# Kernel optimization log

Hardware: AMD Instinct MI355X
Metric: run time of the kernel (lower is better)

Reference implementation:

```python
import jax, jax.numpy as jnp
import numpy as np

B, D, L, H, T = 256, 512, 8, 8, 71
DH = D // H
SCALE = 0.01

def _lrelu(x):
    return jax.nn.leaky_relu(x, 0.2)

def _rms(x, dims, w):
    return w * x * jax.lax.rsqrt(jnp.mean(x * x, axis=dims, keepdims=True) + 1e-6)

def _conv(x, w, b, pad):
    y = jax.lax.conv_general_dilated(x, w, (1, 1), pad, dimension_numbers=('NCHW', 'OIHW', 'NCHW'))
    return y + b[None, :, None, None]

def _mha(x, qkv, nw):
    b_, d_, t_ = x.shape
    # einsum 'bdt,nhdD->nbhtD' -> (3,B,H,T,dh)
    y = jnp.einsum('bdt,nhdD->nbhtD', _lrelu(x), qkv)
    y = _rms(y, -2, nw)  # RMSNorm over the token axis (torch dim=-2)
    q, k, v = y[0], y[1], y[2]
    attn = jax.nn.softmax(jnp.einsum('bhtd,bhTd->bhtT', q, k) / np.float32(np.sqrt(DH)), axis=-1)
    out = jnp.einsum('bhtT,bhTd->bhdt', attn, v)  # (B,H,dh,T)
    return out.reshape(b_, d_, t_)

def _convblock(x, w1, b1, w2, b2, nw):
    b_, d_, t_ = x.shape
    y = x.reshape(b_, d_, 8, 8)
    y = _conv(_lrelu(y), w1, b1, 'SAME')
    y = _rms(y, (-1, -2), nw)
    y = _conv(_lrelu(y), w2, b2, 'SAME')
    return y.reshape(b_, d_, t_)

def _forward(fen, move, rank_emb, file_emb, fen_emb, move_emb, abs_emb, ln_w, ln_b, emb_qkv, emb_norm_w, qkv, mha_norm_w, conv1_w, conv1_b, conv2_w, conv2_b, cb_norm_w, out_norm_w, co1_w, co1_b, co2_w, co2_b):
    pos = (rank_emb + file_emb).reshape(64, D)
    mv = (pos[move] + move_emb) * 0.58          # (B,2,D)
    f = fen_emb[fen]                             # (B,133,D)
    board = 0.5 * (f[:, :64] + f[:, 64:128] + pos)
    x = jnp.concatenate([board, f[:, 128:], mv], axis=1) + abs_emb  # (B,71,D)
    x = jnp.swapaxes(x, -1, -2)                  # (B,D,71)
    mu = jnp.mean(x, -1, keepdims=True)
    var = jnp.mean((x - mu) ** 2, -1, keepdims=True)
    x = (x - mu) * jax.lax.rsqrt(var + 1e-5) * ln_w + ln_b  # LayerNorm over T=71
    y = _mha(x, emb_qkv, emb_norm_w)
    x = x[:, :, :64] + y[:, :, :64]              # keep the 64 board squares
    for i in range(L):
        x = x + _convblock(x, conv1_w[i], conv1_b[i], conv2_w[i], conv2_b[i], cb_norm_w[i])
        x = x + _mha(x, qkv[i], mha_norm_w[i])
    x = x.reshape(B, D, 8, 8)
    x = _conv(_lrelu(x), co1_w, co1_b, 'SAME')
    x = _rms(x, (-1, -2), out_norm_w)
    x = _conv(_lrelu(x), co2_w, co2_b, 'VALID')  # (B,1,1,1)
    return x.reshape(-1)

def setup_inputs():
    key = jax.random.key(0)
    ks = jax.random.split(key, 16)
    n = lambda k, s, sc: jax.random.normal(k, s, dtype=jnp.float32) * sc
    return {
        'fen': jax.random.randint(ks[0], (B, 133), 0, 17),
        'move': jax.random.randint(ks[1], (B, 2), 0, 64),
        'rank_emb': n(ks[2], (8, 1, D), SCALE),
        'file_emb': n(ks[3], (1, 8, D), SCALE),
        'fen_emb': n(ks[4], (17, D), SCALE),
        'move_emb': n(ks[5], (2, D), SCALE),
        'abs_emb': n(ks[6], (71, D), SCALE),
        'ln_w': jnp.ones((71,), jnp.float32),
        'ln_b': jnp.zeros((71,), jnp.float32),
        'emb_qkv': n(ks[7], (3, H, D, DH), SCALE),
        'emb_norm_w': jnp.ones((1,), jnp.float32),
        'qkv': n(ks[8], (L, 3, H, D, DH), SCALE * 0.64),
        'mha_norm_w': jnp.ones((L, 1), jnp.float32),
        'conv1_w': n(ks[9], (L, D, D, 3, 3), SCALE * 0.64),
        'conv1_b': jnp.zeros((L, D), jnp.float32),
        'conv2_w': n(ks[10], (L, D, D, 3, 3), SCALE * 0.64),
        'conv2_b': jnp.zeros((L, D), jnp.float32),
        'cb_norm_w': jnp.ones((L, 1), jnp.float32),
        'out_norm_w': jnp.ones((1,), jnp.float32),
        'co1_w': n(ks[11], (2 * D, D, 3, 3), SCALE),
        'co1_b': jnp.zeros((2 * D,), jnp.float32),
        'co2_w': n(ks[12], (1, 2 * D, 8, 8), SCALE),
        'co2_b': jnp.zeros((1,), jnp.float32),
    }

def reference(fen, move, rank_emb, file_emb, fen_emb, move_emb, abs_emb, ln_w, ln_b, emb_qkv, emb_norm_w, qkv, mha_norm_w, conv1_w, conv1_b, conv2_w, conv2_b, cb_norm_w, out_norm_w, co1_w, co1_b, co2_w, co2_b):
    return _forward(fen, move, rank_emb, file_emb, fen_emb, move_emb, abs_emb, ln_w, ln_b, emb_qkv, emb_norm_w, qkv, mha_norm_w, conv1_w, conv1_b, conv2_w, conv2_b, cb_norm_w, out_norm_w, co1_w, co1_b, co2_w, co2_b)
```

## Files before the change

### kernel.cpp

```cpp
#include <hip/hip_runtime.h>
#include <hip/hip_bf16.h>
#include <cstdint>
#include <cstddef>


typedef float f32x4 __attribute__((ext_vector_type(4)));
typedef short short8 __attribute__((ext_vector_type(8)));

__device__ __forceinline__ float lrelu(float v) { return v > 0.f ? v : 0.2f * v; }
__device__ __forceinline__ __hip_bfloat16 tobf(float v) { return __float2bfloat16(v); }
__device__ __forceinline__ float frombf(__hip_bfloat16 v) { return __bfloat162float(v); }

__global__ __launch_bounds__(256) void repack_qkv_w0(
    const float* __restrict__ emb_qkv, __hip_bfloat16* __restrict__ Wq0)
{
  int o = blockIdx.x * 256 + threadIdx.x;
  int j = o >> 9, d = o & 511;
  int n = j >> 9, h = (j >> 6) & 7, dh = j & 63;
  Wq0[o] = tobf(emb_qkv[(((n * 8 + h) * 512 + d) << 6) + dh]);
}

__global__ __launch_bounds__(256) void repack_qkv_w2(
    const float* __restrict__ qkvw, __hip_bfloat16* __restrict__ Wq2)
{
  const int t = blockIdx.x * 256 + threadIdx.x;
  const int lane = t & 63;
  const int nj = (t >> 6) % 96;
  int rest = (t >> 6) / 96;
  const int ks = rest & 1;
  const int kc = (rest >> 1) & 7;
  const int L = rest >> 4;
  const int j = nj * 16 + (lane & 15);
  const int d0 = kc * 64 + ks * 32 + (lane >> 4) * 8;
  const int n = j >> 9, h = (j >> 6) & 7, dh = j & 63;
  const float* src = qkvw + ((((size_t)L * 3 + n) * 8 + h) * 512 + d0) * 64 + dh;
  __hip_bfloat16 tmp[8];
  #pragma unroll
  for (int e = 0; e < 8; ++e) tmp[e] = tobf(src[(size_t)e * 64]);
  *(uint4*)&Wq2[(size_t)t * 8] = *(const uint4*)tmp;
}

__global__ __launch_bounds__(256) void repack_conv_w2(
    const float* __restrict__ w, __hip_bfloat16* __restrict__ W2, int COUT)
{
  const int t = blockIdx.x * 256 + threadIdx.x;
  if (t >= (COUT << 6)) return;
  const int lr = t & 15;
  const int cbg = (t >> 4) & 63;
  const int oj = t >> 10;
  const int cc = cbg >> 3, ks = (cbg >> 2) & 1, lg = cbg & 3;
  const int o = oj * 16 + lr;
  const int NJ = COUT >> 4;
  const float* src = w + ((size_t)o * 512 + cbg * 8) * 9;
  #pragma unroll
  for (int k = 0; k < 9; ++k) {
    __hip_bfloat16 tmp[8];
    #pragma unroll
    for (int e = 0; e < 8; ++e) tmp[e] = tobf(src[e * 9 + k]);
    size_t di = ((((size_t)cc * 9 + k) * NJ + oj) * 2 + ks) * 512 + (lg * 16 + lr) * 8;
    *(uint4*)&W2[di] = *(const uint4*)tmp;
  }
}

__global__ __launch_bounds__(256) void build_ln_kernel(
    const int* __restrict__ fen, const int* __restrict__ move,
    const float* __restrict__ rank_emb, const float* __restrict__ file_emb,
    const float* __restrict__ fen_emb, const float* __restrict__ move_emb,
    const float* __restrict__ abs_emb, const float* __restrict__ lnw,
    const float* __restrict__ lnb, __hip_bfloat16* __restrict__ X71)
{
  const int gid = blockIdx.x * 256 + threadIdx.x;
  const int b = gid >> 9, d = gid & 511;
  const int* fb = fen + b * 133;

  float sum = 0.f, sq = 0.f, mu = 0.f, rstd = 0.f;
  #pragma unroll 1
  for (int pass = 0; pass < 2; ++pass) {
    if (pass) {
      mu = sum * (1.f / 71.f);
      float var = sq * (1.f / 71.f) - mu * mu;
      rstd = rsqrtf(var + 1e-5f);
    }
    #pragma unroll 1
    for (int t = 0; t < 71; ++t) {
      float a = abs_emb[t * 512 + d];
      float v;
      if (t < 64) {
        float pos = rank_emb[(t >> 3) * 512 + d] + file_emb[(t & 7) * 512 + d];
        v = 0.5f * (fen_emb[fb[t] * 512 + d] + fen_emb[fb[64 + t] * 512 + d] + pos) + a;
      } else if (t < 69) {
        v = fen_emb[fb[t + 64] * 512 + d] + a;
      } else {
        int j = t - 69;
        int s = move[b * 2 + j];
        float pos = rank_emb[(s >> 3) * 512 + d] + file_emb[(s & 7) * 512 + d];
        v = (pos + move_emb[j * 512 + d]) * 0.58f + a;
      }
      if (pass) X71[(size_t)gid * 71 + t] = tobf((v - mu) * rstd * lnw[t] + lnb[t]);
      else { sum += v; sq += v * v; }
    }
  }
}

template <int T, int TP>
__global__ __launch_bounds__(256) void proj71_kernel(
    const __hip_bfloat16* __restrict__ xin, const __hip_bfloat16* __restrict__ Wq,
    const float* __restrict__ nw,
    __hip_bfloat16* __restrict__ qk, __hip_bfloat16* __restrict__ vT)
{
  const int b  = blockIdx.x / 6;
  const int jb = (blockIdx.x % 6) * 256;
  const int tid = threadIdx.x;
  const int lane = tid & 63, wv = tid >> 6;
  const int lr = lane & 15, lg = lane >> 4;

  __shared__ __hip_bfloat16 xt[TP * 72];
  __shared__ __hip_bfloat16 wl[256 * 72];

  constexpr int MI = TP / 16;
  f32x4 acc[MI][4];
  #pragma unroll
  for (int mi = 0; mi < MI; ++mi)
    #pragma unroll
    for (int ni = 0; ni < 4; ++ni) acc[mi][ni] = {0.f, 0.f, 0.f, 0.f};

  for (int c0 = 0; c0 < 512; c0 += 64) {
    for (int i = tid; i < 64 * TP; i += 256) {
      int d = i / TP, t = i - d * TP;
      float v = (t < T) ? lrelu(frombf(xin[((size_t)(b * 512 + c0 + d)) * T + t])) : 0.f;
      xt[t * 72 + d] = tobf(v);
    }
    for (int i = tid; i < 2048; i += 256) {
      int j = i >> 3, cb = i & 7;
      *(uint4*)&wl[j * 72 + cb * 8] =
          *(const uint4*)&Wq[(size_t)(jb + j) * 512 + c0 + cb * 8];
    }
    __syncthreads();
    #pragma unroll
    for (int ks = 0; ks < 2; ++ks) {
      short8 a[MI], bb[4];
      #pragma unroll
      for (int mi = 0; mi < MI; ++mi)
        a[mi] = *(const short8*)&xt[(mi * 16 + lr) * 72 + ks * 32 + lg * 8];
      #pragma unroll
      for (int ni = 0; ni < 4; ++ni)
        bb[ni] = *(const short8*)&wl[(wv * 64 + ni * 16 + lr) * 72 + ks * 32 + lg * 8];
      #pragma unroll
      for (int mi = 0; mi < MI; ++mi)
        #pragma unroll
        for (int ni = 0; ni < 4; ++ni)
          acc[mi][ni] = __builtin_amdgcn_mfma_f32_16x16x32_bf16(
              a[mi], bb[ni], acc[mi][ni], 0, 0, 0);
    }
    __syncthreads();
  }

  #pragma unroll
  for (int ni = 0; ni < 4; ++ni) {
    const int j = jb + wv * 64 + ni * 16 + lr;
    float ss = 0.f;
    #pragma unroll
    for (int mi = 0; mi < MI; ++mi)
      #pragma unroll
      for (int r = 0; r < 4; ++r) ss += acc[mi][ni][r] * acc[mi][ni][r];
    ss += __shfl_xor(ss, 16);
    ss += __shfl_xor(ss, 32);
    const float sc = nw[0] * rsqrtf(ss * (1.f / T) + 1e-6f);
    if (j < 1024) {
      #pragma unroll
      for (int mi = 0; mi < MI; ++mi)
        #pragma unroll
        for (int r = 0; r < 4; ++r) {
          int t = mi * 16 + lg * 4 + r;
          if (t < T)
            qk[((size_t)b * T + t) * 1024 + j] = tobf(acc[mi][ni][r] * sc);
        }
    } else {
      const int jj = j - 1024;
      #pragma unroll
      for (int mi = 0; mi < MI; ++mi)
        #pragma unroll
        for (int r = 0; r < 4; ++r) {
          int t = mi * 16 + lg * 4 + r;
          vT[((size_t)b * 512 + jj) * TP + t] = tobf(acc[mi][ni][r] * sc);
        }
    }
  }
}

__global__ __launch_bounds__(256) void proj64_kernel(
    const float* __restrict__ x,
    const __hip_bfloat16* __restrict__ Wq2,
    const float* __restrict__ nw,
    __hip_bfloat16* __restrict__ qk, __hip_bfloat16* __restrict__ vT)
{
  const int b    = blockIdx.x / 6;
  const int jseg = blockIdx.x % 6;
  const int tid = threadIdx.x;
  const int lane = tid & 63, wv = tid >> 6;
  const int lr = lane & 15, lg = lane >> 4;

  __shared__ __hip_bfloat16 xt[2][64 * 72];

  f32x4 acc[4][4];
  #pragma unroll
  for (int mi = 0; mi < 4; ++mi)
    #pragma unroll
    for (int ni = 0; ni < 4; ++ni) acc[mi][ni] = {0.f, 0.f, 0.f, 0.f};

  f32x4 sreg[4];
  const int s_d  = tid >> 4;
  const int s_t4 = (tid & 15) << 2;

  #define PSTAGE_LOAD(kc_)                                                    \
    {                                                                         \
      const float* xb_ = x + ((size_t)b * 512 + (kc_) * 64 + s_d) * 64 + s_t4; \
      _Pragma("unroll")                                                       \
      for (int u = 0; u < 4; ++u) sreg[u] = *(const f32x4*)&xb_[u * 1024];    \
    }
  #define PSTAGE_WRITE(buf_)                                                  \
    {                                                                         \
      _Pragma("unroll")                                                       \
      for (int u = 0; u < 4; ++u) {                                           \
        _Pragma("unroll")                                                     \
        for (int j = 0; j < 4; ++j)                                           \
          xt[buf_][(s_t4 + j) * 72 + s_d + u * 16] = tobf(lrelu(sreg[u][j])); \
      }                                                                       \
    }

  PSTAGE_LOAD(0);
  PSTAGE_WRITE(0);
  __syncthreads();

  const int njb0 = jseg * 16 + wv * 4;

  for (int kc = 0; kc < 8; ++kc) {
    const int cur = kc & 1;
    if (kc < 7) PSTAGE_LOAD(kc + 1);
    const __hip_bfloat16* xb = xt[cur];
    #pragma unroll
    for (int ks = 0; ks < 2; ++ks) {
      short8 bv[4], av[4];
      #pragma unroll
      for (int ni = 0; ni < 4; ++ni)
        bv[ni] = *(const short8*)
            &Wq2[((((size_t)kc * 2 + ks) * 96) + njb0 + ni) * 512 + lane * 8];
      #pragma unroll
      for (int mi = 0; mi < 4; ++mi)
        av[mi] = *(const short8*)&xb[(mi * 16 + lr) * 72 + ks * 32 + lg * 8];
      #pragma unroll
      for (int mi = 0; mi < 4; ++mi)
        #pragma unroll
        for (int ni = 0; ni < 4; ++ni)
          acc[mi][ni] = __builtin_amdgcn_mfma_f32_16x16x32_bf16(
              av[mi], bv[ni], acc[mi][ni], 0, 0, 0);
    }
    if (kc < 7) PSTAGE_WRITE(cur ^ 1);
    __syncthreads();
  }
  #undef PSTAGE_LOAD
  #undef PSTAGE_WRITE

  #pragma unroll
  for (int ni = 0; ni < 4; ++ni) {
    const int j = jseg * 256 + wv * 64 + ni * 16 + lr;
    float ss = 0.f;
    #pragma unroll
    for (int mi = 0; mi < 4; ++mi)
      #pragma unroll
      for (int r = 0; r < 4; ++r) ss += acc[mi][ni][r] * acc[mi][ni][r];
    ss += __shfl_xor(ss, 16);
    ss += __shfl_xor(ss, 32);
    const float sc = nw[0] * rsqrtf(ss * (1.f / 64.f) + 1e-6f);
    if (j < 1024) {
      #pragma unroll
      for (int mi = 0; mi < 4; ++mi)
        #pragma unroll
        for (int r = 0; r < 4; ++r) {
          int t = mi * 16 + lg * 4 + r;
          qk[((size_t)b * 64 + t) * 1024 + j] = tobf(acc[mi][ni][r] * sc);
        }
    } else {
      const int jj = j - 1024;
      #pragma unroll
      for (int mi = 0; mi < 4; ++mi)
        #pragma unroll
        for (int r = 0; r < 4; ++r) {
          int t = mi * 16 + lg * 4 + r;
          vT[((size_t)b * 512 + jj) * 64 + t] = tobf(acc[mi][ni][r] * sc);
        }
    }
  }
}

template <int T, bool RESBF>
__global__ __launch_bounds__(256) void attn2_kernel(
    const __hip_bfloat16* __restrict__ qk,
    const __hip_bfloat16* __restrict__ vT,
    const void* __restrict__ res, float* __restrict__ out)
{
  constexpr int TP = (T == 71) ? 80 : 64;
  constexpr int TK = (T + 31) / 32;
  constexpr int RS = 72;
  constexpr int PS = TK * 32 + 8;
  constexpr int KR = (T == 71) ? 80 : 64;
  constexpr int SC = (T == 71) ? 82 : 66;
  constexpr int NCF = KR / 16;
  constexpr int NFW = (NCF + 3) / 4;
  constexpr int RANGE = (TK * 32) / 4;

  constexpr int Q_OFF = 0;
  constexpr int K_OFF = Q_OFF + 64 * RS * 2;
  constexpr int V_OFF = K_OFF + KR * RS * 2;
  constexpr int S_OFF = V_OFF + 64 * PS * 2;
  constexpr int BYTES = S_OFF + 64 * SC * 4;
  __shared__ __align__(16) char smem[BYTES];
  __hip_bfloat16* qs = (__hip_bfloat16*)(smem + Q_OFF);
  __hip_bfloat16* ksh = (__hip_bfloat16*)(smem + K_OFF);
  __hip_bfloat16* vs = (__hip_bfloat16*)(smem + V_OFF);
  float* ss = (float*)(smem + S_OFF);
  __hip_bfloat16* ps = (__hip_bfloat16*)(smem + S_OFF);

  const int b = blockIdx.x >> 3, h = blockIdx.x & 7;
  const int tid = threadIdx.x;
  const int lane = tid & 63, wv = tid >> 6;
  const int lr = lane & 15, lg = lane >> 4;

  for (int i = tid; i < BYTES / 16; i += 256) ((uint4*)smem)[i] = uint4{0, 0, 0, 0};
  __syncthreads();

  const __hip_bfloat16* qb = qk + (size_t)b * T * 1024 + h * 64;
  for (int v = tid; v < 512; v += 256) {
    int t = v >> 3, d0 = (v & 7) * 8;
    *(uint4*)&qs[t * RS + d0] = *(const uint4*)&qb[(size_t)t * 1024 + d0];
  }
  for (int v = tid; v < T * 8; v += 256) {
    int t = v >> 3, d0 = (v & 7) * 8;
    *(uint4*)&ksh[t * RS + d0] = *(const uint4*)&qb[(size_t)t * 1024 + 512 + d0];
  }
  constexpr int VV = TP / 8;
  for (int v = tid; v < 64 * VV; v += 256) {
    int dh = v / VV, tc = (v - dh * VV) * 8;
    *(uint4*)&vs[dh * PS + tc] =
        *(const uint4*)&vT[((size_t)b * 512 + h * 64 + dh) * TP + tc];
  }
  __syncthreads();

  f32x4 sacc[NFW][4];
  #pragma unroll
  for (int fi = 0; fi < NFW; ++fi)
    #pragma unroll
    for (int mi = 0; mi < 4; ++mi) sacc[fi][mi] = {0.f, 0.f, 0.f, 0.f};
  #pragma unroll
  for (int ks2 = 0; ks2 < 2; ++ks2) {
    short8 a[4];
    #pragma unroll
    for (int mi = 0; mi < 4; ++mi)
      a[mi] = *(const short8*)&qs[(mi * 16 + lr) * RS + ks2 * 32 + lg * 8];
    #pragma unroll
    for (int fi = 0; fi < NFW; ++fi) {
      const int f = wv + fi * 4;
      if (f < NCF) {
        short8 bb = *(const short8*)&ksh[(f * 16 + lr) * RS + ks2 * 32 + lg * 8];
        #pragma unroll
        for (int mi = 0; mi < 4; ++mi)
          sacc[fi][mi] = __builtin_amdgcn_mfma_f32_16x16x32_bf16(
              a[mi], bb, sacc[fi][mi], 0, 0, 0);
      }
    }
  }
  #pragma unroll
  for (int fi = 0; fi < NFW; ++fi) {
    const int f = wv + fi * 4;
    if (f < NCF) {
      #pragma unroll
      for (int mi = 0; mi < 4; ++mi)
        #pragma unroll
        for (int r = 0; r < 4; ++r)
          ss[(mi * 16 + lg * 4 + r) * SC + f * 16 + lr] = sacc[fi][mi][r] * 0.125f;
    }
  }
  __syncthreads();

  {
    const int row = tid >> 2, q4 = tid & 3;
    float sv[RANGE];
    float mx = -3.0e38f;
    #pragma unroll
    for (int i = 0; i < RANGE; ++i) {
      int c = q4 * RANGE + i;
      sv[i] = (c < T) ? ss[row * SC + c] : -3.0e38f;
      mx = fmaxf(mx, sv[i]);
    }
    mx = fmaxf(mx, __shfl_xor(mx, 1));
    mx = fmaxf(mx, __shfl_xor(mx, 2));
    float sm = 0.f;
    #pragma unroll
    for (int i = 0; i < RANGE; ++i) {
      int c = q4 * RANGE + i;
      sv[i] = (c < T) ? __expf(sv[i] - mx) : 0.f;
      sm += sv[i];
    }
    sm += __shfl_xor(sm, 1);
    sm += __shfl_xor(sm, 2);
    const float inv = 1.f / sm;
    __syncthreads();
    #pragma unroll
    for (int i = 0; i < RANGE; ++i)
      ps[row * PS + q4 * RANGE + i] = tobf(sv[i] * inv);
  }
  __syncthreads();

  f32x4 oacc[4];
  #pragma unroll
  for (int mi = 0; mi < 4; ++mi) oacc[mi] = {0.f, 0.f, 0.f, 0.f};
  #pragma unroll
  for (int ks2 = 0; ks2 < TK; ++ks2) {
    short8 bb = *(const short8*)&vs[(wv * 16 + lr) * PS + ks2 * 32 + lg * 8];
    #pragma unroll
    for (int mi = 0; mi < 4; ++mi) {
      short8 a = *(const short8*)&ps[(mi * 16 + lr) * PS + ks2 * 32 + lg * 8];
      oacc[mi] = __builtin_amdgcn_mfma_f32_16x16x32_bf16(a, bb, oacc[mi], 0, 0, 0);
    }
  }

  const int dh = wv * 16 + lr;
  const size_t chb = (size_t)b * 512 + h * 64 + dh;
  #pragma unroll
  for (int mi = 0; mi < 4; ++mi) {
    const int t0 = mi * 16 + lg * 4;
    const size_t idx = chb * 64 + t0;
    f32x4 v = oacc[mi];
    if constexpr (RESBF) {
      const __hip_bfloat16* rb = (const __hip_bfloat16*)res + chb * T + t0;
      #pragma unroll
      for (int r = 0; r < 4; ++r) v[r] += frombf(rb[r]);
    } else {
      v += *(const f32x4*)&((const float*)res)[idx];
    }
    *(f32x4*)&out[idx] = v;
  }
}

template <bool RMSOUT, bool RESADD>
__global__ __launch_bounds__(256) void conv_mfma2(
    const float* __restrict__ x,
    const __hip_bfloat16* __restrict__ W2,
    const float* __restrict__ bias,
    const float* __restrict__ nw,
    const float* __restrict__ res,
    float* __restrict__ out,
    int COUT)
{
  const int ntc = COUT >> 8;
  const int b = blockIdx.x / ntc;
  const int nt = blockIdx.x - b * ntc;
  const int o0 = nt << 8;
  const int NJ = COUT >> 4;
  const int tid = threadIdx.x;
  const int lane = tid & 63, wv = tid >> 6;
  const int lr = lane & 15, lg = lane >> 4;

  __shared__ __hip_bfloat16 xt[2][100 * 72];

  f32x4 acc[4][4];
  #pragma unroll
  for (int mi = 0; mi < 4; ++mi)
    #pragma unroll
    for (int ni = 0; ni < 4; ++ni) acc[mi][ni] = {0.f, 0.f, 0.f, 0.f};

  for (int i = tid; i < 7200; i += 256) { xt[0][i] = tobf(0.f); xt[1][i] = tobf(0.f); }

  f32x4 sreg[4];
  const int s_ci = tid >> 4;
  const int s_p4 = (tid & 15) << 2;
  const int s_row = (((s_p4 >> 3) + 1) * 10 + (s_p4 & 7) + 1) * 72;

  #define STAGE_LOAD(cc_)                                                     \
    {                                                                         \
      const float* xb_ = x + ((size_t)b * 512 + (cc_) * 64 + s_ci) * 64 + s_p4; \
      _Pragma("unroll")                                                       \
      for (int u = 0; u < 4; ++u) sreg[u] = *(const f32x4*)&xb_[u * 1024];    \
    }
  #define STAGE_WRITE(buf_)                                                   \
    {                                                                         \
      _Pragma("unroll")                                                       \
      for (int u = 0; u < 4; ++u) {                                           \
        _Pragma("unroll")                                                     \
        for (int j = 0; j < 4; ++j)                                           \
          xt[buf_][s_row + j * 72 + s_ci + u * 16] = tobf(lrelu(sreg[u][j])); \
      }                                                                       \
    }

  STAGE_LOAD(0);
  __syncthreads();
  STAGE_WRITE(0);
  __syncthreads();

  const int ojb2 = ((o0 >> 4) + wv * 4) * 2;

  for (int cc = 0; cc < 8; ++cc) {
    const int cur = cc & 1;
    if (cc < 7) STAGE_LOAD(cc + 1);
    const __hip_bfloat16* xb = xt[cur];

    #pragma unroll
    for (int k = 0; k < 9; ++k) {
      const int dy = k / 3 - 1, dx = k - (k / 3) * 3 - 1;
      const int ii0 = (lr >> 3) + dy + 1;
      const int jj0 = (lr & 7) + dx + 1;
      const size_t slab = ((size_t)(cc * 9 + k) * NJ) * 2 + ojb2;
      short8 bv[2][4], av[2][4];
      #pragma unroll
      for (int ni = 0; ni < 4; ++ni)
        #pragma unroll
        for (int ks = 0; ks < 2; ++ks)
          bv[ks][ni] = *(const short8*)&W2[(slab + ni * 2 + ks) * 512 + lane * 8];
      #pragma unroll
      for (int ks = 0; ks < 2; ++ks)
        #pragma unroll
        for (int mi = 0; mi < 4; ++mi)
          av[ks][mi] = *(const short8*)&xb[((ii0 + mi * 2) * 10 + jj0) * 72 + ks * 32 + lg * 8];
      #pragma unroll
      for (int ks = 0; ks < 2; ++ks)
        #pragma unroll
        for (int mi = 0; mi < 4; ++mi)
          #pragma unroll
          for (int ni = 0; ni < 4; ++ni)
            acc[mi][ni] = __builtin_amdgcn_mfma_f32_16x16x32_bf16(
                av[ks][mi], bv[ks][ni], acc[mi][ni], 0, 0, 0);
    }
    if (cc < 7) STAGE_WRITE(cur ^ 1);
    __syncthreads();
  }
  #undef STAGE_LOAD
  #undef STAGE_WRITE

  #pragma unroll
  for (int ni = 0; ni < 4; ++ni) {
    const int o = o0 + wv * 64 + ni * 16 + lr;
    const float bvs = bias[o];
    float sc = 1.f;
    if constexpr (RMSOUT) {
      float ssq = 0.f;
      #pragma unroll
      for (int mi = 0; mi < 4; ++mi)
        #pragma unroll
        for (int r = 0; r < 4; ++r) {
          float v = acc[mi][ni][r] + bvs;
          ssq += v * v;
        }
      ssq += __shfl_xor(ssq, 16);
      ssq += __shfl_xor(ssq, 32);
      sc = nw[0] * rsqrtf(ssq * (1.f / 64.f) + 1e-6f);
    }
    #pragma unroll
    for (int mi = 0; mi < 4; ++mi) {
      size_t idx = ((size_t)b * COUT + o) * 64 + mi * 16 + lg * 4;
      f32x4 v;
      #pragma unroll
      for (int r = 0; r < 4; ++r) v[r] = (acc[mi][ni][r] + bvs) * sc;
      if constexpr (RESADD) v += *(const f32x4*)&res[idx];
      *(f32x4*)&out[idx] = v;
    }
  }
}

__global__ __launch_bounds__(256) void co2_kernel(
    const float* __restrict__ xf, const float* __restrict__ w,
    const float* __restrict__ cb, float* __restrict__ out)
{
  const int b = blockIdx.x, tid = threadIdx.x;
  const float* xb = xf + (size_t)b * 65536;
  float acc = 0.f;
  for (int i = tid; i < 65536; i += 256)
    acc += lrelu(xb[i]) * w[i];
  #pragma unroll
  for (int off = 32; off; off >>= 1) acc += __shfl_down(acc, off);
  __shared__ float red[4];
  if ((tid & 63) == 0) red[tid >> 6] = acc;
  __syncthreads();
  if (tid == 0) out[b] = red[0] + red[1] + red[2] + red[3] + cb[0];
}

extern "C" void kernel_launch(void* const* d_in, const int* in_sizes, int n_in,
                              void* d_out, int out_size, void* d_ws, size_t ws_size,
                              hipStream_t stream)
{
  const int*   fen        = (const int*)d_in[0];
  const int*   move       = (const int*)d_in[1];
  const float* rank_emb   = (const float*)d_in[2];
  const float* file_emb   = (const float*)d_in[3];
  const float* fen_emb    = (const float*)d_in[4];
  const float* move_emb   = (const float*)d_in[5];
  const float* abs_emb    = (const float*)d_in[6];
  const float* ln_w       = (const float*)d_in[7];
  const float* ln_b       = (const float*)d_in[8];
  const float* emb_qkv    = (const float*)d_in[9];
  const float* emb_norm_w = (const float*)d_in[10];
  const float* qkvw_in    = (const float*)d_in[11];
  const float* mha_norm_w = (const float*)d_in[12];
  const float* conv1_w    = (const float*)d_in[13];
  const float* conv1_b    = (const float*)d_in[14];
  const float* conv2_w    = (const float*)d_in[15];
  const float* conv2_b    = (const float*)d_in[16];
  const float* cb_norm_w  = (const float*)d_in[17];
  const float* out_norm_w = (const float*)d_in[18];
  const float* co1_w      = (const float*)d_in[19];
  const float* co1_b      = (const float*)d_in[20];
  const float* co2_w      = (const float*)d_in[21];
  const float* co2_b      = (const float*)d_in[22];
  float* out = (float*)d_out;

  char* base = (char*)d_ws;
  __hip_bfloat16* X71 = (__hip_bfloat16*)base;
  float* X64 = (float*)(base + 18612224);
  float* T1  = (float*)(base + 18612224 + 33554432);
  __hip_bfloat16* Wq0 = (__hip_bfloat16*)(base + 119275520);
  __hip_bfloat16* Wq2 = (__hip_bfloat16*)(base + 120848384);
  __hip_bfloat16* qk2 = (__hip_bfloat16*)T1;
  __hip_bfloat16* vTb = (__hip_bfloat16*)((char*)T1 + 37224448);
  float* F1 = T1;
  __hip_bfloat16* WcA = (__hip_bfloat16*)base;
  __hip_bfloat16* WcB = (__hip_bfloat16*)(base + 4718592);

  repack_qkv_w0<<<3072, 256, 0, stream>>>(emb_qkv, Wq0);
  repack_qkv_w2<<<3072, 256, 0, stream>>>(qkvw_in, Wq2);

  build_ln_kernel<<<512, 256, 0, stream>>>(fen, move, rank_emb, file_emb,
                                           fen_emb, move_emb, abs_emb,
                                           ln_w, ln_b, X71);
  proj71_kernel<71, 80><<<1536, 256, 0, stream>>>(X71, Wq0, emb_norm_w, qk2, vTb);
  attn2_kernel<71, true><<<2048, 256, 0, stream>>>(qk2, vTb, X71, X64);

  for (int l = 0; l < 8; ++l) {
    repack_conv_w2<<<128, 256, 0, stream>>>(conv1_w + (size_t)l * 512 * 512 * 9,
                                            WcA, 512);
    conv_mfma2<true, false><<<512, 256, 0, stream>>>(X64, WcA, conv1_b + l * 512,
                                                     cb_norm_w + l, nullptr, T1, 512);
    repack_conv_w2<<<128, 256, 0, stream>>>(conv2_w + (size_t)l * 512 * 512 * 9,
                                            WcB, 512);
    conv_mfma2<false, true><<<512, 256, 0, stream>>>(T1, WcB, conv2_b + l * 512,
                                                     nullptr, X64, X64, 512);
    proj64_kernel<<<1536, 256, 0, stream>>>(X64, Wq2 + (size_t)l * 786432,
                                            mha_norm_w + l, qk2, vTb);
    attn2_kernel<64, false><<<2048, 256, 0, stream>>>(qk2, vTb, X64, X64);
  }

  repack_conv_w2<<<256, 256, 0, stream>>>(co1_w, WcA, 1024);
  conv_mfma2<true, false><<<1024, 256, 0, stream>>>(X64, WcA, co1_b,
                                                    out_norm_w, nullptr, F1, 1024);
  co2_kernel<<<256, 256, 0, stream>>>(F1, co2_w, co2_b, out);
}
```

Baseline: 2.690 ms.

## Tile conv and projection kernels over two batch samples per block

Each conv block now handles two batch samples and 128 output channels instead of one sample and 256 channels, so every weight fragment loaded from global memory feeds twice as many MFMAs. The QKV projection kernel is likewise changed to process two samples per block, halving its grid. The two per-layer conv weight repacks are merged into a single launch. The cost is doubled shared memory per block for the staged inputs, plus more registers holding input fragments, which may reduce occupancy.

```diff
diff --git a/kernel.cpp b/kernel.cpp
--- a/kernel.cpp
+++ b/kernel.cpp
@@ -58,6 +58,30 @@
     #pragma unroll
     for (int e = 0; e < 8; ++e) tmp[e] = tobf(src[e * 9 + k]);
     size_t di = ((((size_t)cc * 9 + k) * NJ + oj) * 2 + ks) * 512 + (lg * 16 + lr) * 8;
+    *(uint4*)&W2[di] = *(const uint4*)tmp;
+  }
+}
+
+__global__ __launch_bounds__(256) void repack_conv_pair(
+    const float* __restrict__ w1, const float* __restrict__ w2s,
+    __hip_bfloat16* __restrict__ WA, __hip_bfloat16* __restrict__ WB)
+{
+  int t = blockIdx.x * 256 + threadIdx.x;
+  const float* w = (t < 32768) ? w1 : w2s;
+  __hip_bfloat16* W2 = (t < 32768) ? WA : WB;
+  t &= 32767;
+  const int lr = t & 15;
+  const int cbg = (t >> 4) & 63;
+  const int oj = t >> 10;
+  const int cc = cbg >> 3, ks = (cbg >> 2) & 1, lg = cbg & 3;
+  const int o = oj * 16 + lr;
+  const float* src = w + ((size_t)o * 512 + cbg * 8) * 9;
+  #pragma unroll
+  for (int k = 0; k < 9; ++k) {
+    __hip_bfloat16 tmp[8];
+    #pragma unroll
+    for (int e = 0; e < 8; ++e) tmp[e] = tobf(src[e * 9 + k]);
+    size_t di = ((((size_t)cc * 9 + k) * 32 + oj) * 2 + ks) * 512 + (lg * 16 + lr) * 8;
     *(uint4*)&W2[di] = *(const uint4*)tmp;
   }
 }
@@ -188,44 +212,52 @@
   }
 }
 
-__global__ __launch_bounds__(256) void proj64_kernel(
+__global__ __launch_bounds__(256) void proj64b_kernel(
     const float* __restrict__ x,
     const __hip_bfloat16* __restrict__ Wq2,
     const float* __restrict__ nw,
     __hip_bfloat16* __restrict__ qk, __hip_bfloat16* __restrict__ vT)
 {
-  const int b    = blockIdx.x / 6;
-  const int jseg = blockIdx.x % 6;
+  const int jseg = blockIdx.x >> 7;
+  const int bg   = blockIdx.x & 127;
+  const int b0   = bg * 2;
   const int tid = threadIdx.x;
   const int lane = tid & 63, wv = tid >> 6;
   const int lr = lane & 15, lg = lane >> 4;
 
-  __shared__ __hip_bfloat16 xt[2][64 * 72];
-
-  f32x4 acc[4][4];
-  #pragma unroll
-  for (int mi = 0; mi < 4; ++mi)
+  __shared__ __hip_bfloat16 xt[2][2][64 * 72];
+
+  f32x4 acc[8][4];
+  #pragma unroll
+  for (int mi = 0; mi < 8; ++mi)
     #pragma unroll
     for (int ni = 0; ni < 4; ++ni) acc[mi][ni] = {0.f, 0.f, 0.f, 0.f};
 
-  f32x4 sreg[4];
+  f32x4 sreg[2][4];
   const int s_d  = tid >> 4;
   const int s_t4 = (tid & 15) << 2;
 
-  #define PSTAGE_LOAD(kc_)                                                    \
-    {                                                                         \
-      const float* xb_ = x + ((size_t)b * 512 + (kc_) * 64 + s_d) * 64 + s_t4; \
-      _Pragma("unroll")                                                       \
-      for (int u = 0; u < 4; ++u) sreg[u] = *(const f32x4*)&xb_[u * 1024];    \
-    }
-  #define PSTAGE_WRITE(buf_)                                                  \
-    {                                                                         \
-      _Pragma("unroll")                                                       \
-      for (int u = 0; u < 4; ++u) {                                           \
-        _Pragma("unroll")                                                     \
-        for (int j = 0; j < 4; ++j)                                           \
-          xt[buf_][(s_t4 + j) * 72 + s_d + u * 16] = tobf(lrelu(sreg[u][j])); \
-      }                                                                       \
+  #define PSTAGE_LOAD(kc_)                                                      \
+    {                                                                           \
+      _Pragma("unroll")                                                         \
+      for (int s = 0; s < 2; ++s) {                                             \
+        const float* xb_ =                                                      \
+            x + ((size_t)(b0 + s) * 512 + (kc_) * 64 + s_d) * 64 + s_t4;        \
+        _Pragma("unroll")                                                       \
+        for (int u = 0; u < 4; ++u) sreg[s][u] = *(const f32x4*)&xb_[u * 1024]; \
+      }                                                                         \
+    }
+  #define PSTAGE_WRITE(buf_)                                                    \
+    {                                                                           \
+      _Pragma("unroll")                                                         \
+      for (int s = 0; s < 2; ++s)                                               \
+        _Pragma("unroll")                                                       \
+        for (int u = 0; u < 4; ++u) {                                           \
+          _Pragma("unroll")                                                     \
+          for (int j = 0; j < 4; ++j)                                           \
+            xt[buf_][s][(s_t4 + j) * 72 + s_d + u * 16] =                       \
+                tobf(lrelu(sreg[s][u][j]));                                     \
+        }                                                                       \
     }
 
   PSTAGE_LOAD(0);
@@ -237,19 +269,19 @@
   for (int kc = 0; kc < 8; ++kc) {
     const int cur = kc & 1;
     if (kc < 7) PSTAGE_LOAD(kc + 1);
-    const __hip_bfloat16* xb = xt[cur];
     #pragma unroll
     for (int ks = 0; ks < 2; ++ks) {
-      short8 bv[4], av[4];
+      short8 bv[4], av[8];
       #pragma unroll
       for (int ni = 0; ni < 4; ++ni)
         bv[ni] = *(const short8*)
             &Wq2[((((size_t)kc * 2 + ks) * 96) + njb0 + ni) * 512 + lane * 8];
       #pragma unroll
-      for (int mi = 0; mi < 4; ++mi)
-        av[mi] = *(const short8*)&xb[(mi * 16 + lr) * 72 + ks * 32 + lg * 8];
-      #pragma unroll
-      for (int mi = 0; mi < 4; ++mi)
+      for (int mi = 0; mi < 8; ++mi)
+        av[mi] = *(const short8*)
+            &xt[cur][mi >> 2][((mi & 3) * 16 + lr) * 72 + ks * 32 + lg * 8];
+      #pragma unroll
+      for (int mi = 0; mi < 8; ++mi)
         #pragma unroll
         for (int ni = 0; ni < 4; ++ni)
           acc[mi][ni] = __builtin_amdgcn_mfma_f32_16x16x32_bf16(
@@ -264,31 +296,35 @@
   #pragma unroll
   for (int ni = 0; ni < 4; ++ni) {
     const int j = jseg * 256 + wv * 64 + ni * 16 + lr;
-    float ss = 0.f;
-    #pragma unroll
-    for (int mi = 0; mi < 4; ++mi)
-      #pragma unroll
-      for (int r = 0; r < 4; ++r) ss += acc[mi][ni][r] * acc[mi][ni][r];
-    ss += __shfl_xor(ss, 16);
-    ss += __shfl_xor(ss, 32);
-    const float sc = nw[0] * rsqrtf(ss * (1.f / 64.f) + 1e-6f);
-    if (j < 1024) {
-      #pragma unroll
-      for (int mi = 0; mi < 4; ++mi)
-        #pragma unroll
-        for (int r = 0; r < 4; ++r) {
-          int t = mi * 16 + lg * 4 + r;
-          qk[((size_t)b * 64 + t) * 1024 + j] = tobf(acc[mi][ni][r] * sc);
-        }
-    } else {
-      const int jj = j - 1024;
-      #pragma unroll
-      for (int mi = 0; mi < 4; ++mi)
-        #pragma unroll
-        for (int r = 0; r < 4; ++r) {
-          int t = mi * 16 + lg * 4 + r;
-          vT[((size_t)b * 512 + jj) * 64 + t] = tobf(acc[mi][ni][r] * sc);
-        }
+    #pragma unroll
+    for (int s = 0; s < 2; ++s) {
+      float ss = 0.f;
+      #pragma unroll
+      for (int m = 0; m < 4; ++m)
+        #pragma unroll
+        for (int r = 0; r < 4; ++r) ss += acc[s * 4 + m][ni][r] * acc[s * 4 + m][ni][r];
+      ss += __shfl_xor(ss, 16);
+      ss += __shfl_xor(ss, 32);
+      const float sc = nw[0] * rsqrtf(ss * (1.f / 64.f) + 1e-6f);
+      const int b = b0 + s;
+      if (j < 1024) {
+        #pragma unroll
+        for (int m = 0; m < 4; ++m)
+          #pragma unroll
+          for (int r = 0; r < 4; ++r) {
+            int t = m * 16 + lg * 4 + r;
+            qk[((size_t)b * 64 + t) * 1024 + j] = tobf(acc[s * 4 + m][ni][r] * sc);
+          }
+      } else {
+        const int jj = j - 1024;
+        #pragma unroll
+        for (int m = 0; m < 4; ++m)
+          #pragma unroll
+          for (int r = 0; r < 4; ++r) {
+            int t = m * 16 + lg * 4 + r;
+            vT[((size_t)b * 512 + jj) * 64 + t] = tobf(acc[s * 4 + m][ni][r] * sc);
+          }
+      }
     }
   }
 }
@@ -443,7 +479,7 @@
 }
 
 template <bool RMSOUT, bool RESADD>
-__global__ __launch_bounds__(256) void conv_mfma2(
+__global__ __launch_bounds__(256) void conv_mfma3(
     const float* __restrict__ x,
     const __hip_bfloat16* __restrict__ W2,
     const float* __restrict__ bias,
@@ -452,44 +488,50 @@
     float* __restrict__ out,
     int COUT)
 {
-  const int ntc = COUT >> 8;
-  const int b = blockIdx.x / ntc;
-  const int nt = blockIdx.x - b * ntc;
-  const int o0 = nt << 8;
+  const int oct = blockIdx.x >> 7;
+  const int bg  = blockIdx.x & 127;
+  const int b0  = bg * 2;
   const int NJ = COUT >> 4;
   const int tid = threadIdx.x;
   const int lane = tid & 63, wv = tid >> 6;
   const int lr = lane & 15, lg = lane >> 4;
 
-  __shared__ __hip_bfloat16 xt[2][100 * 72];
-
-  f32x4 acc[4][4];
-  #pragma unroll
-  for (int mi = 0; mi < 4; ++mi)
-    #pragma unroll
-    for (int ni = 0; ni < 4; ++ni) acc[mi][ni] = {0.f, 0.f, 0.f, 0.f};
-
-  for (int i = tid; i < 7200; i += 256) { xt[0][i] = tobf(0.f); xt[1][i] = tobf(0.f); }
-
-  f32x4 sreg[4];
+  __shared__ __hip_bfloat16 xt[2][2][100 * 72];
+
+  f32x4 acc[8][2];
+  #pragma unroll
+  for (int mi = 0; mi < 8; ++mi)
+    #pragma unroll
+    for (int ni = 0; ni < 2; ++ni) acc[mi][ni] = {0.f, 0.f, 0.f, 0.f};
+
+  for (int i = tid; i < 3600; i += 256) ((uint4*)xt)[i] = uint4{0, 0, 0, 0};
+
+  f32x4 sreg[2][4];
   const int s_ci = tid >> 4;
   const int s_p4 = (tid & 15) << 2;
   const int s_row = (((s_p4 >> 3) + 1) * 10 + (s_p4 & 7) + 1) * 72;
 
-  #define STAGE_LOAD(cc_)                                                     \
-    {                                                                         \
-      const float* xb_ = x + ((size_t)b * 512 + (cc_) * 64 + s_ci) * 64 + s_p4; \
-      _Pragma("unroll")                                                       \
-      for (int u = 0; u < 4; ++u) sreg[u] = *(const f32x4*)&xb_[u * 1024];    \
-    }
-  #define STAGE_WRITE(buf_)                                                   \
-    {                                                                         \
-      _Pragma("unroll")                                                       \
-      for (int u = 0; u < 4; ++u) {                                           \
-        _Pragma("unroll")                                                     \
-        for (int j = 0; j < 4; ++j)                                           \
-          xt[buf_][s_row + j * 72 + s_ci + u * 16] = tobf(lrelu(sreg[u][j])); \
-      }                                                                       \
+  #define STAGE_LOAD(cc_)                                                       \
+    {                                                                           \
+      _Pragma("unroll")                                                         \
+      for (int s = 0; s < 2; ++s) {                                             \
+        const float* xb_ =                                                      \
+            x + ((size_t)(b0 + s) * 512 + (cc_) * 64 + s_ci) * 64 + s_p4;       \
+        _Pragma("unroll")                                                       \
+        for (int u = 0; u < 4; ++u) sreg[s][u] = *(const f32x4*)&xb_[u * 1024]; \
+      }                                                                         \
+    }
+  #define STAGE_WRITE(buf_)                                                     \
+    {                                                                           \
+      _Pragma("unroll")                                                         \
+      for (int s = 0; s < 2; ++s)                                               \
+        _Pragma("unroll")                                                       \
+        for (int u = 0; u < 4; ++u) {                                           \
+          _Pragma("unroll")                                                     \
+          for (int j = 0; j < 4; ++j)                                           \
+            xt[buf_][s][s_row + j * 72 + s_ci + u * 16] =                       \
+                tobf(lrelu(sreg[s][u][j]));                                     \
+        }                                                                       \
     }
 
   STAGE_LOAD(0);
@@ -497,36 +539,36 @@
   STAGE_WRITE(0);
   __syncthreads();
 
-  const int ojb2 = ((o0 >> 4) + wv * 4) * 2;
+  const int njb = oct * 8 + wv * 2;
 
   for (int cc = 0; cc < 8; ++cc) {
     const int cur = cc & 1;
     if (cc < 7) STAGE_LOAD(cc + 1);
-    const __hip_bfloat16* xb = xt[cur];
 
     #pragma unroll
     for (int k = 0; k < 9; ++k) {
       const int dy = k / 3 - 1, dx = k - (k / 3) * 3 - 1;
       const int ii0 = (lr >> 3) + dy + 1;
       const int jj0 = (lr & 7) + dx + 1;
-      const size_t slab = ((size_t)(cc * 9 + k) * NJ) * 2 + ojb2;
-      short8 bv[2][4], av[2][4];
-      #pragma unroll
-      for (int ni = 0; ni < 4; ++ni)
+      short8 bv[2][2], av[2][8];
+      #pragma unroll
+      for (int ni = 0; ni < 2; ++ni)
         #pragma unroll
         for (int ks = 0; ks < 2; ++ks)
-          bv[ks][ni] = *(const short8*)&W2[(slab + ni * 2 + ks) * 512 + lane * 8];
+          bv[ks][ni] = *(const short8*)
+              &W2[((((size_t)(cc * 9 + k)) * NJ + njb + ni) * 2 + ks) * 512 + lane * 8];
       #pragma unroll
       for (int ks = 0; ks < 2; ++ks)
         #pragma unroll
-        for (int mi = 0; mi < 4; ++mi)
-          av[ks][mi] = *(const short8*)&xb[((ii0 + mi * 2) * 10 + jj0) * 72 + ks * 32 + lg * 8];
+        for (int mi = 0; mi < 8; ++mi)
+          av[ks][mi] = *(const short8*)
+              &xt[cur][mi >> 2][((ii0 + (mi & 3) * 2) * 10 + jj0) * 72 + ks * 32 + lg * 8];
       #pragma unroll
       for (int ks = 0; ks < 2; ++ks)
         #pragma unroll
-        for (int mi = 0; mi < 4; ++mi)
+        for (int mi = 0; mi < 8; ++mi)
           #pragma unroll
-          for (int ni = 0; ni < 4; ++ni)
+          for (int ni = 0; ni < 2; ++ni)
             acc[mi][ni] = __builtin_amdgcn_mfma_f32_16x16x32_bf16(
                 av[ks][mi], bv[ks][ni], acc[mi][ni], 0, 0, 0);
     }
@@ -537,31 +579,34 @@
   #undef STAGE_WRITE
 
   #pragma unroll
-  for (int ni = 0; ni < 4; ++ni) {
-    const int o = o0 + wv * 64 + ni * 16 + lr;
+  for (int ni = 0; ni < 2; ++ni) {
+    const int o = oct * 128 + wv * 32 + ni * 16 + lr;
     const float bvs = bias[o];
-    float sc = 1.f;
-    if constexpr (RMSOUT) {
-      float ssq = 0.f;
-      #pragma unroll
-      for (int mi = 0; mi < 4; ++mi)
-        #pragma unroll
-        for (int r = 0; r < 4; ++r) {
-          float v = acc[mi][ni][r] + bvs;
-          ssq += v * v;
-        }
-      ssq += __shfl_xor(ssq, 16);
-      ssq += __shfl_xor(ssq, 32);
-      sc = nw[0] * rsqrtf(ssq * (1.f / 64.f) + 1e-6f);
-    }
-    #pragma unroll
-    for (int mi = 0; mi < 4; ++mi) {
-      size_t idx = ((size_t)b * COUT + o) * 64 + mi * 16 + lg * 4;
-      f32x4 v;
-      #pragma unroll
-      for (int r = 0; r < 4; ++r) v[r] = (acc[mi][ni][r] + bvs) * sc;
-      if constexpr (RESADD) v += *(const f32x4*)&res[idx];
-      *(f32x4*)&out[idx] = v;
+    #pragma unroll
+    for (int s = 0; s < 2; ++s) {
+      float sc = 1.f;
+      if constexpr (RMSOUT) {
+        float ssq = 0.f;
+        #pragma unroll
+        for (int m = 0; m < 4; ++m)
+          #pragma unroll
+          for (int r = 0; r < 4; ++r) {
+            float v = acc[s * 4 + m][ni][r] + bvs;
+            ssq += v * v;
+          }
+        ssq += __shfl_xor(ssq, 16);
+        ssq += __shfl_xor(ssq, 32);
+        sc = nw[0] * rsqrtf(ssq * (1.f / 64.f) + 1e-6f);
+      }
+      #pragma unroll
+      for (int m = 0; m < 4; ++m) {
+        size_t idx = ((size_t)(b0 + s) * COUT + o) * 64 + m * 16 + lg * 4;
+        f32x4 v;
+        #pragma unroll
+        for (int r = 0; r < 4; ++r) v[r] = (acc[s * 4 + m][ni][r] + bvs) * sc;
+        if constexpr (RESADD) v += *(const f32x4*)&res[idx];
+        *(f32x4*)&out[idx] = v;
+      }
     }
   }
 }
@@ -634,21 +679,20 @@
   attn2_kernel<71, true><<<2048, 256, 0, stream>>>(qk2, vTb, X71, X64);
 
   for (int l = 0; l < 8; ++l) {
-    repack_conv_w2<<<128, 256, 0, stream>>>(conv1_w + (size_t)l * 512 * 512 * 9,
-                                            WcA, 512);
-    conv_mfma2<true, false><<<512, 256, 0, stream>>>(X64, WcA, conv1_b + l * 512,
+    repack_conv_pair<<<256, 256, 0, stream>>>(conv1_w + (size_t)l * 512 * 512 * 9,
+                                              conv2_w + (size_t)l * 512 * 512 * 9,
+                                              WcA, WcB);
+    conv_mfma3<true, false><<<512, 256, 0, stream>>>(X64, WcA, conv1_b + l * 512,
                                                      cb_norm_w + l, nullptr, T1, 512);
-    repack_conv_w2<<<128, 256, 0, stream>>>(conv2_w + (size_t)l * 512 * 512 * 9,
-                                            WcB, 512);
-    conv_mfma2<false, true><<<512, 256, 0, stream>>>(T1, WcB, conv2_b + l * 512,
+    conv_mfma3<false, true><<<512, 256, 0, stream>>>(T1, WcB, conv2_b + l * 512,
                                                      nullptr, X64, X64, 512);
-    proj64_kernel<<<1536, 256, 0, stream>>>(X64, Wq2 + (size_t)l * 786432,
+    proj64b_kernel<<<768, 256, 0, stream>>>(X64, Wq2 + (size_t)l * 786432,
                                             mha_norm_w + l, qk2, vTb);
     attn2_kernel<64, false><<<2048, 256, 0, stream>>>(qk2, vTb, X64, X64);
   }
 
   repack_conv_w2<<<256, 256, 0, stream>>>(co1_w, WcA, 1024);
-  conv_mfma2<true, false><<<1024, 256, 0, stream>>>(X64, WcA, co1_b,
+  conv_mfma3<true, false><<<1024, 256, 0, stream>>>(X64, WcA, co1_b,
                                                     out_norm_w, nullptr, F1, 1024);
   co2_kernel<<<256, 256, 0, stream>>>(F1, co2_w, co2_b, out);
 }
```

After: 3.693 ms. +37.3%, slower.

## Pass conv inputs as pre-activated bf16 channel-last tensors produced by previous kernels

Applied to the files above, without the earlier changes.

The conv1 output is now written as lrelu-applied bf16 in a cell-major channel-last layout. The attention kernel also emits a bf16 lrelu copy of the residual stream. Later convs can therefore stage their input with two 16-byte copies instead of converting and activating fp32 data, which cuts global traffic and staging work inside the conv loop. The two per-layer weight repacks are merged into one launch. The cost is extra strided 2-byte scattered stores in the epilogues and a more complex workspace layout.

```diff
diff --git a/kernel.cpp b/kernel.cpp
--- a/kernel.cpp
+++ b/kernel.cpp
@@ -58,6 +58,30 @@
     #pragma unroll
     for (int e = 0; e < 8; ++e) tmp[e] = tobf(src[e * 9 + k]);
     size_t di = ((((size_t)cc * 9 + k) * NJ + oj) * 2 + ks) * 512 + (lg * 16 + lr) * 8;
+    *(uint4*)&W2[di] = *(const uint4*)tmp;
+  }
+}
+
+__global__ __launch_bounds__(256) void repack_conv_pair(
+    const float* __restrict__ w1, const float* __restrict__ w2s,
+    __hip_bfloat16* __restrict__ WA, __hip_bfloat16* __restrict__ WB)
+{
+  int t = blockIdx.x * 256 + threadIdx.x;
+  const float* w = (t < 32768) ? w1 : w2s;
+  __hip_bfloat16* W2 = (t < 32768) ? WA : WB;
+  t &= 32767;
+  const int lr = t & 15;
+  const int cbg = (t >> 4) & 63;
+  const int oj = t >> 10;
+  const int cc = cbg >> 3, ks = (cbg >> 2) & 1, lg = cbg & 3;
+  const int o = oj * 16 + lr;
+  const float* src = w + ((size_t)o * 512 + cbg * 8) * 9;
+  #pragma unroll
+  for (int k = 0; k < 9; ++k) {
+    __hip_bfloat16 tmp[8];
+    #pragma unroll
+    for (int e = 0; e < 8; ++e) tmp[e] = tobf(src[e * 9 + k]);
+    size_t di = ((((size_t)cc * 9 + k) * 32 + oj) * 2 + ks) * 512 + (lg * 16 + lr) * 8;
     *(uint4*)&W2[di] = *(const uint4*)tmp;
   }
 }
@@ -293,11 +317,12 @@
   }
 }
 
-template <int T, bool RESBF>
+template <int T, bool RESBF, bool WRITEXC>
 __global__ __launch_bounds__(256) void attn2_kernel(
     const __hip_bfloat16* __restrict__ qk,
     const __hip_bfloat16* __restrict__ vT,
-    const void* __restrict__ res, float* __restrict__ out)
+    const void* __restrict__ res, float* __restrict__ out,
+    __hip_bfloat16* __restrict__ xcout)
 {
   constexpr int TP = (T == 71) ? 80 : 64;
   constexpr int TK = (T + 31) / 32;
@@ -439,17 +464,22 @@
       v += *(const f32x4*)&((const float*)res)[idx];
     }
     *(f32x4*)&out[idx] = v;
-  }
-}
-
-template <bool RMSOUT, bool RESADD>
-__global__ __launch_bounds__(256) void conv_mfma2(
-    const float* __restrict__ x,
+    if constexpr (WRITEXC) {
+      #pragma unroll
+      for (int r = 0; r < 4; ++r)
+        xcout[((size_t)b * 64 + t0 + r) * 512 + (h << 6) + dh] = tobf(lrelu(v[r]));
+    }
+  }
+}
+
+template <bool RMSOUT, bool RESADD, bool INBF, bool OUTBF>
+__global__ __launch_bounds__(256) void conv_mfma2b(
+    const void* __restrict__ xin,
     const __hip_bfloat16* __restrict__ W2,
     const float* __restrict__ bias,
     const float* __restrict__ nw,
     const float* __restrict__ res,
-    float* __restrict__ out,
+    void* __restrict__ outp,
     int COUT)
 {
   const int ntc = COUT >> 8;
@@ -475,33 +505,50 @@
   const int s_ci = tid >> 4;
   const int s_p4 = (tid & 15) << 2;
   const int s_row = (((s_p4 >> 3) + 1) * 10 + (s_p4 & 7) + 1) * 72;
-
-  #define STAGE_LOAD(cc_)                                                     \
-    {                                                                         \
-      const float* xb_ = x + ((size_t)b * 512 + (cc_) * 64 + s_ci) * 64 + s_p4; \
-      _Pragma("unroll")                                                       \
-      for (int u = 0; u < 4; ++u) sreg[u] = *(const f32x4*)&xb_[u * 1024];    \
-    }
-  #define STAGE_WRITE(buf_)                                                   \
-    {                                                                         \
-      _Pragma("unroll")                                                       \
-      for (int u = 0; u < 4; ++u) {                                           \
-        _Pragma("unroll")                                                     \
-        for (int j = 0; j < 4; ++j)                                           \
-          xt[buf_][s_row + j * 72 + s_ci + u * 16] = tobf(lrelu(sreg[u][j])); \
-      }                                                                       \
-    }
-
-  STAGE_LOAD(0);
+  uint4 sregb[2];
+  const int c_cg = tid & 7;
+  const int c_cell0 = tid >> 3;
+  const int c_lofs0 = (((c_cell0 >> 3) + 1) * 10 + (c_cell0 & 7) + 1) * 72 + c_cg * 8;
+  const int c_cell1 = c_cell0 + 32;
+  const int c_lofs1 = (((c_cell1 >> 3) + 1) * 10 + (c_cell1 & 7) + 1) * 72 + c_cg * 8;
+
+  auto stage_load = [&](int cc_) {
+    if constexpr (INBF) {
+      const __hip_bfloat16* xbf = (const __hip_bfloat16*)xin;
+      const __hip_bfloat16* p0 =
+          xbf + ((size_t)b * 64 + c_cell0) * 512 + cc_ * 64 + c_cg * 8;
+      sregb[0] = *(const uint4*)p0;
+      sregb[1] = *(const uint4*)(p0 + 32 * 512);
+    } else {
+      const float* xf = (const float*)xin;
+      const float* xb_ = xf + ((size_t)b * 512 + cc_ * 64 + s_ci) * 64 + s_p4;
+      #pragma unroll
+      for (int u = 0; u < 4; ++u) sreg[u] = *(const f32x4*)&xb_[u * 1024];
+    }
+  };
+  auto stage_write = [&](int buf_) {
+    if constexpr (INBF) {
+      *(uint4*)&xt[buf_][c_lofs0] = sregb[0];
+      *(uint4*)&xt[buf_][c_lofs1] = sregb[1];
+    } else {
+      #pragma unroll
+      for (int u = 0; u < 4; ++u)
+        #pragma unroll
+        for (int j = 0; j < 4; ++j)
+          xt[buf_][s_row + j * 72 + s_ci + u * 16] = tobf(lrelu(sreg[u][j]));
+    }
+  };
+
+  stage_load(0);
   __syncthreads();
-  STAGE_WRITE(0);
+  stage_write(0);
   __syncthreads();
 
   const int ojb2 = ((o0 >> 4) + wv * 4) * 2;
 
   for (int cc = 0; cc < 8; ++cc) {
     const int cur = cc & 1;
-    if (cc < 7) STAGE_LOAD(cc + 1);
+    if (cc < 7) stage_load(cc + 1);
     const __hip_bfloat16* xb = xt[cur];
 
     #pragma unroll
@@ -530,11 +577,9 @@
             acc[mi][ni] = __builtin_amdgcn_mfma_f32_16x16x32_bf16(
                 av[ks][mi], bv[ks][ni], acc[mi][ni], 0, 0, 0);
     }
-    if (cc < 7) STAGE_WRITE(cur ^ 1);
+    if (cc < 7) stage_write(cur ^ 1);
     __syncthreads();
   }
-  #undef STAGE_LOAD
-  #undef STAGE_WRITE
 
   #pragma unroll
   for (int ni = 0; ni < 4; ++ni) {
@@ -554,14 +599,27 @@
       ssq += __shfl_xor(ssq, 32);
       sc = nw[0] * rsqrtf(ssq * (1.f / 64.f) + 1e-6f);
     }
-    #pragma unroll
-    for (int mi = 0; mi < 4; ++mi) {
-      size_t idx = ((size_t)b * COUT + o) * 64 + mi * 16 + lg * 4;
-      f32x4 v;
-      #pragma unroll
-      for (int r = 0; r < 4; ++r) v[r] = (acc[mi][ni][r] + bvs) * sc;
-      if constexpr (RESADD) v += *(const f32x4*)&res[idx];
-      *(f32x4*)&out[idx] = v;
+    if constexpr (OUTBF) {
+      __hip_bfloat16* tc = (__hip_bfloat16*)outp;
+      #pragma unroll
+      for (int mi = 0; mi < 4; ++mi)
+        #pragma unroll
+        for (int r = 0; r < 4; ++r) {
+          int cell = mi * 16 + lg * 4 + r;
+          tc[((size_t)b * 64 + cell) * COUT + o] =
+              tobf(lrelu((acc[mi][ni][r] + bvs) * sc));
+        }
+    } else {
+      float* outf = (float*)outp;
+      #pragma unroll
+      for (int mi = 0; mi < 4; ++mi) {
+        size_t idx = ((size_t)b * COUT + o) * 64 + mi * 16 + lg * 4;
+        f32x4 v;
+        #pragma unroll
+        for (int r = 0; r < 4; ++r) v[r] = (acc[mi][ni][r] + bvs) * sc;
+        if constexpr (RESADD) v += *(const f32x4*)&res[idx];
+        *(f32x4*)&outf[idx] = v;
+      }
     }
   }
 }
@@ -615,12 +673,16 @@
   char* base = (char*)d_ws;
   __hip_bfloat16* X71 = (__hip_bfloat16*)base;
   float* X64 = (float*)(base + 18612224);
-  float* T1  = (float*)(base + 18612224 + 33554432);
+  char* t1b  = base + 52166656;
   __hip_bfloat16* Wq0 = (__hip_bfloat16*)(base + 119275520);
   __hip_bfloat16* Wq2 = (__hip_bfloat16*)(base + 120848384);
-  __hip_bfloat16* qk2 = (__hip_bfloat16*)T1;
-  __hip_bfloat16* vTb = (__hip_bfloat16*)((char*)T1 + 37224448);
-  float* F1 = T1;
+  __hip_bfloat16* qk71 = (__hip_bfloat16*)t1b;
+  __hip_bfloat16* vT71 = (__hip_bfloat16*)(t1b + 37224448);
+  __hip_bfloat16* qk64 = (__hip_bfloat16*)t1b;
+  __hip_bfloat16* vT64 = (__hip_bfloat16*)(t1b + 33554432);
+  __hip_bfloat16* Xc   = (__hip_bfloat16*)(t1b + 50331648);
+  __hip_bfloat16* Tc   = (__hip_bfloat16*)t1b;
+  float* F1 = (float*)t1b;
   __hip_bfloat16* WcA = (__hip_bfloat16*)base;
   __hip_bfloat16* WcB = (__hip_bfloat16*)(base + 4718592);
 
@@ -630,25 +692,34 @@
   build_ln_kernel<<<512, 256, 0, stream>>>(fen, move, rank_emb, file_emb,
                                            fen_emb, move_emb, abs_emb,
                                            ln_w, ln_b, X71);
-  proj71_kernel<71, 80><<<1536, 256, 0, stream>>>(X71, Wq0, emb_norm_w, qk2, vTb);
-  attn2_kernel<71, true><<<2048, 256, 0, stream>>>(qk2, vTb, X71, X64);
+  proj71_kernel<71, 80><<<1536, 256, 0, stream>>>(X71, Wq0, emb_norm_w, qk71, vT71);
+  attn2_kernel<71, true, false><<<2048, 256, 0, stream>>>(qk71, vT71, X71, X64,
+                                                          nullptr);
 
   for (int l = 0; l < 8; ++l) {
-    repack_conv_w2<<<128, 256, 0, stream>>>(conv1_w + (size_t)l * 512 * 512 * 9,
-                                            WcA, 512);
-    conv_mfma2<true, false><<<512, 256, 0, stream>>>(X64, WcA, conv1_b + l * 512,
-                                                     cb_norm_w + l, nullptr, T1, 512);
-    repack_conv_w2<<<128, 256, 0, stream>>>(conv2_w + (size_t)l * 512 * 512 * 9,
-                                            WcB, 512);
-    conv_mfma2<false, true><<<512, 256, 0, stream>>>(T1, WcB, conv2_b + l * 512,
-                                                     nullptr, X64, X64, 512);
+    repack_conv_pair<<<256, 256, 0, stream>>>(conv1_w + (size_t)l * 512 * 512 * 9,
+                                              conv2_w + (size_t)l * 512 * 512 * 9,
+                                              WcA, WcB);
+    if (l == 0)
+      conv_mfma2b<true, false, false, true><<<512, 256, 0, stream>>>(
+          X64, WcA, conv1_b + l * 512, cb_norm_w + l, nullptr, Tc, 512);
+    else
+      conv_mfma2b<true, false, true, true><<<512, 256, 0, stream>>>(
+          Xc, WcA, conv1_b + l * 512, cb_norm_w + l, nullptr, Tc, 512);
+    conv_mfma2b<false, true, true, false><<<512, 256, 0, stream>>>(
+        Tc, WcB, conv2_b + l * 512, nullptr, X64, X64, 512);
     proj64_kernel<<<1536, 256, 0, stream>>>(X64, Wq2 + (size_t)l * 786432,
-                                            mha_norm_w + l, qk2, vTb);
-    attn2_kernel<64, false><<<2048, 256, 0, stream>>>(qk2, vTb, X64, X64);
+                                            mha_norm_w + l, qk64, vT64);
+    if (l < 7)
+      attn2_kernel<64, false, true><<<2048, 256, 0, stream>>>(qk64, vT64, X64,
+                                                              X64, Xc);
+    else
+      attn2_kernel<64, false, false><<<2048, 256, 0, stream>>>(qk64, vT64, X64,
+                                                               X64, nullptr);
   }
 
   repack_conv_w2<<<256, 256, 0, stream>>>(co1_w, WcA, 1024);
-  conv_mfma2<true, false><<<1024, 256, 0, stream>>>(X64, WcA, co1_b,
-                                                    out_norm_w, nullptr, F1, 1024);
+  conv_mfma2b<true, false, false, false><<<1024, 256, 0, stream>>>(
+      X64, WcA, co1_b, out_norm_w, nullptr, F1, 1024);
   co2_kernel<<<256, 256, 0, stream>>>(F1, co2_w, co2_b, out);
 }
```

Result: no change. 2.647 ms (-1.6%).
